# Optimization experiments

Hardware: AMD Instinct MI355X
Metric: run time of the kernel (lower is better)

## Reference

```python
import jax, jax.numpy as jnp
import numpy as np
import math

B, N, E, H = 2, 1024, 768, 12
D = E // H  # head_size = 64


def setup_inputs() -> dict:
    key = jax.random.key(0)
    ks = jax.random.split(key, 12)
    node_features = jax.random.normal(ks[0], (B, N, E), dtype=jnp.float32)
    adj = jax.random.bernoulli(ks[1], 0.5, (B, N, N))
    # ensure every row has at least one edge (self-loop) to avoid NaN softmax rows
    adj = adj | jnp.eye(N, dtype=bool)[None]
    key_edge_features = jax.random.normal(ks[2], (B, N, N, D), dtype=jnp.float32)
    s = 1.0 / math.sqrt(E)
    Wq = jax.random.normal(ks[3], (E, E), dtype=jnp.float32) * s
    bq = jnp.zeros((E,), dtype=jnp.float32)
    Wk = jax.random.normal(ks[4], (E, E), dtype=jnp.float32) * s
    bk = jnp.zeros((E,), dtype=jnp.float32)
    Wv = jax.random.normal(ks[5], (E, E), dtype=jnp.float32) * s
    bv = jnp.zeros((E,), dtype=jnp.float32)
    Wo = jax.random.normal(ks[6], (E, E), dtype=jnp.float32) * s
    bo = jnp.zeros((E,), dtype=jnp.float32)
    return dict(node_features=node_features, adj=adj, key_edge_features=key_edge_features,
                Wq=Wq, bq=bq, Wk=Wk, bk=bk, Wv=Wv, bv=bv, Wo=Wo, bo=bo)


def _heads(x):
    # (B, N, E) -> (B, H, N, D)
    return x.reshape(B, N, H, D).transpose(0, 2, 1, 3)


def reference(node_features, adj, key_edge_features, Wq, bq, Wk, bk, Wv, bv, Wo, bo):
    Q = _heads(node_features @ Wq.T + bq)  # (B,H,N,D)
    K = _heads(node_features @ Wk.T + bk)
    V = _heads(node_features @ Wv.T + bv)
    scores = jnp.einsum('bhnd,bhmd->bhnm', Q, K)
    scores = scores + jnp.einsum('bhnd,bnmd->bhnm', Q, key_edge_features)
    scores = scores / jnp.sqrt(jnp.float32(E))  # NOTE: sqrt(embed_dim), faithful to source
    scores = jnp.where(adj[:, None, :, :], scores, -jnp.inf)
    probs = jax.nn.softmax(scores, axis=-1)
    out = jnp.einsum('bhnm,bhmd->bhnd', probs, V)  # (B,H,N,D)
    out = out.transpose(0, 2, 1, 3).reshape(B, N, E)
    return out @ Wo.T + bo
```

## Files before the change

### kernel.cpp

```cpp
#include <hip/hip_runtime.h>
#include <hip/hip_bf16.h>
#include <cstdint>

typedef __attribute__((ext_vector_type(8))) short s16x8;
typedef __attribute__((ext_vector_type(8))) unsigned short u16x8_t;
typedef __attribute__((ext_vector_type(4))) float f32x4_t;
typedef __attribute__((ext_vector_type(4))) unsigned int u32x4_t;
typedef __attribute__((ext_vector_type(4))) unsigned short u16x4_t;

__device__ __forceinline__ unsigned short f2b(float f){
  unsigned u = __float_as_uint(f);
  u += 0x7fffu + ((u>>16)&1u);
  return (unsigned short)(u>>16);
}
__device__ __forceinline__ float b2f(unsigned short s){
  return __uint_as_float(((unsigned)s)<<16);
}
__device__ __forceinline__ unsigned cvt_pk_bf16(float lo, float hi){
  unsigned r;
  asm("v_cvt_pk_bf16_f32 %0, %1, %2" : "=v"(r) : "v"(lo), "v"(hi));
  return r;
}

constexpr float INV_SQRT_E = 0.036084391824351615f;
constexpr float LOG2E = 1.4426950408889634f;

__global__ void k_convert(const float* __restrict__ X,
                          const float* __restrict__ Wq, const float* __restrict__ Wk,
                          const float* __restrict__ Wv, const float* __restrict__ Wo,
                          unsigned short* __restrict__ Xb, unsigned short* __restrict__ Wst){
  const int64_t WTOT = (int64_t)3072*768/4;
  const int64_t XTOT = (int64_t)2048*768/4;
  for (int64_t i = (int64_t)blockIdx.x*blockDim.x + threadIdx.x; i < WTOT+XTOT;
       i += (int64_t)gridDim.x*blockDim.x){
    const float* src; unsigned short* dst;
    if (i < WTOT){
      int64_t e4 = i*4;
      int j = (int)(e4/768), k = (int)(e4 - (int64_t)j*768);
      int w = j/768; int jr = j - w*768;
      const float* Wsel = (w==0)? Wq : (w==1)? Wk : (w==2)? Wv : Wo;
      src = Wsel + (int64_t)jr*768 + k;
      dst = Wst + e4;
    } else {
      int64_t t = (i-WTOT)*4;
      src = X + t; dst = Xb + t;
    }
    f32x4_t v = *reinterpret_cast<const f32x4_t*>(src);
    u16x4_t o;
    o[0]=f2b(v[0]); o[1]=f2b(v[1]); o[2]=f2b(v[2]); o[3]=f2b(v[3]);
    *reinterpret_cast<u16x4_t*>(dst) = o;
  }
}

__launch_bounds__(256)
__global__ void k_gemm(const unsigned short* __restrict__ A,
                       const unsigned short* __restrict__ Wst,
                       const int mode,
                       const float* __restrict__ bq, const float* __restrict__ bk,
                       const float* __restrict__ bv, const float* __restrict__ bo,
                       unsigned short* __restrict__ Qb, unsigned short* __restrict__ Kb,
                       unsigned short* __restrict__ Vt, float* __restrict__ Out){
  __shared__ unsigned short As[64*64];
  __shared__ unsigned short Bs[64*64];
  const int tiles_n = (mode==0)?36:12;
  const int tm = blockIdx.x / tiles_n, tn = blockIdx.x % tiles_n;
  const int row0 = tm*64, col0 = tn*64;
  const unsigned short* Bbase = Wst + (mode==0 ? 0 : (int64_t)2304*768);
  const int tid = threadIdx.x;
  const int lane = tid & 63, wvi = tid >> 6;
  const int l15 = lane & 15, lg = lane >> 4;
  const int wr = (wvi>>1)*32, wc = (wvi&1)*32;
  f32x4_t acc[2][2] = {};
  for (int k0=0;k0<768;k0+=64){
    #pragma unroll
    for (int i=0;i<2;i++){
      int t = tid + i*256;
      int r = t>>3, c8 = t&7;
      u32x4_t va = *reinterpret_cast<const u32x4_t*>(A + (int64_t)(row0+r)*768 + k0 + c8*8);
      u32x4_t vb = *reinterpret_cast<const u32x4_t*>(Bbase + (int64_t)(col0+r)*768 + k0 + c8*8);
      int byt = (t*16) ^ ((r&7)<<4);
      *reinterpret_cast<u32x4_t*>(reinterpret_cast<char*>(As)+byt) = va;
      *reinterpret_cast<u32x4_t*>(reinterpret_cast<char*>(Bs)+byt) = vb;
    }
    __syncthreads();
    #pragma unroll
    for (int ks=0;ks<2;ks++){
      s16x8 af[2], bf[2];
      #pragma unroll
      for (int mt=0;mt<2;mt++){
        int r = wr + mt*16 + l15;
        int byt = (r*128 + ks*64 + lg*16) ^ ((r&7)<<4);
        af[mt] = *reinterpret_cast<const s16x8*>(reinterpret_cast<const char*>(As)+byt);
      }
      #pragma unroll
      for (int nt=0;nt<2;nt++){
        int r = wc + nt*16 + l15;
        int byt = (r*128 + ks*64 + lg*16) ^ ((r&7)<<4);
        bf[nt] = *reinterpret_cast<const s16x8*>(reinterpret_cast<const char*>(Bs)+byt);
      }
      #pragma unroll
      for (int mt=0;mt<2;mt++)
        #pragma unroll
        for (int nt=0;nt<2;nt++)
          acc[mt][nt] = __builtin_amdgcn_mfma_f32_16x16x32_bf16(af[mt], bf[nt], acc[mt][nt], 0,0,0);
    }
    __syncthreads();
  }
  #pragma unroll
  for (int mt=0;mt<2;mt++){
    #pragma unroll
    for (int nt=0;nt<2;nt++){
      int j = col0 + wc + nt*16 + l15;
      #pragma unroll
      for (int r=0;r<4;r++){
        int ii = row0 + wr + mt*16 + lg*4 + r;
        float v = acc[mt][nt][r];
        if (mode==0){
          int w = j/768; int e = j - w*768; int h = e>>6, d = e&63;
          int b = ii>>10, n = ii & 1023;
          if (w==0)      Qb[(((int64_t)(b*12+h)*1024)+n)*64+d] = f2b((v + bq[e])*INV_SQRT_E);
          else if (w==1) Kb[(((int64_t)(b*12+h)*1024)+n)*64+d] = f2b(v + bk[e]);
          else           Vt[(((int64_t)(b*12+h)*64)+d)*1024+n] = f2b(v + bv[e]);
        } else {
          Out[(int64_t)ii*768 + j] = v + bo[j];
        }
      }
    }
  }
}

__launch_bounds__(256,2)
__global__ void k_fused(const unsigned short* __restrict__ Qb, const unsigned short* __restrict__ Kb,
                        const unsigned short* __restrict__ Vt, const int* __restrict__ adj,
                        const float* __restrict__ Ef,
                        float* __restrict__ Onum, float* __restrict__ Lws){
  __shared__ float Sk[12][16][36];
  __shared__ unsigned short Sq[16][12][48];
  __shared__ unsigned short Pb[12][16][32];
  const int bid = blockIdx.x;
  const int mh = bid & 7, qt = (bid>>3) & 63, b = bid >> 9;
  const int q0 = qt*16, mbase = mh*128;
  const int tid = threadIdx.x, lane = tid & 63, wvi = tid>>6;
  const int l15 = lane & 15, lg = lane >> 4;
  const int eq = lane >> 2, mg = lane & 3;

  s16x8 afQ[3][2];
  const unsigned short* vB[3];
  const unsigned short* kB[3];
  #pragma unroll
  for (int hh=0;hh<3;hh++){
    const int h = wvi*3+hh;
    const unsigned short* p = Qb + (((int64_t)(b*12+h)*1024) + q0 + l15)*64;
    afQ[hh][0] = *reinterpret_cast<const s16x8*>(p + lg*8);
    afQ[hh][1] = *reinterpret_cast<const s16x8*>(p + 32 + lg*8);
    vB[hh]  = Vt + ((int64_t)(b*12+h)*64)*1024 + mbase + lg*8;
    kB[hh]  = Kb + ((int64_t)(b*12+h)*1024 + mbase + l15)*64;
  }
  s16x8 bfQ[4][2];
  #pragma unroll
  for (int qq=0;qq<4;qq++){
    s16x8 v0 = {}; s16x8 v1 = {};
    if (l15 < 12){
      const unsigned short* p = Qb + (((int64_t)(b*12+l15)*1024) + q0 + wvi*4 + qq)*64;
      v0 = *reinterpret_cast<const s16x8*>(p + lg*8);
      v1 = *reinterpret_cast<const s16x8*>(p + 32 + lg*8);
    }
    bfQ[qq][0]=v0; bfQ[qq][1]=v1;
  }
  const float* efBase = Ef + (((int64_t)b*1024 + q0 + wvi*4)*1024 + mbase + l15)*64 + lg*8;
  const int*  adjBase = adj + ((int64_t)b*1024 + q0 + wvi*4)*1024 + mbase + lg*4;

  f32x4_t accO[3][4] = {};
  float Lp[3] = {0.f,0.f,0.f};

  for (int step=0; step<4; step++){
    const int so = step*32;
    if (step) __syncthreads();
    s16x8 vC[3][4];
    #pragma unroll
    for (int hh=0;hh<3;hh++)
      #pragma unroll
      for (int dsb=0;dsb<4;dsb++)
        vC[hh][dsb] = *reinterpret_cast<const s16x8*>(vB[hh] + (int64_t)(dsb*16+l15)*1024 + so);
    #pragma unroll
    for (int hh=0;hh<3;hh++){
      const int h = wvi*3+hh;
      const unsigned short* kp = kB[hh] + so*64;
      #pragma unroll
      for (int mh2=0;mh2<2;mh2++){
        const unsigned short* kr = kp + mh2*16*64;
        f32x4_t a = {0.f,0.f,0.f,0.f};
        s16x8 k0v = *reinterpret_cast<const s16x8*>(kr + lg*8);
        s16x8 k1v = *reinterpret_cast<const s16x8*>(kr + 32 + lg*8);
        a = __builtin_amdgcn_mfma_f32_16x16x32_bf16(afQ[hh][0], k0v, a, 0,0,0);
        a = __builtin_amdgcn_mfma_f32_16x16x32_bf16(afQ[hh][1], k1v, a, 0,0,0);
        #pragma unroll
        for (int r=0;r<4;r++) Sk[h][lg*4+r][mh2*16+l15] = a[r];
      }
    }
    #pragma unroll
    for (int qq=0;qq<4;qq++){
      const float* ep = efBase + (int64_t)qq*65536 + so*64;
      #pragma unroll
      for (int mt2=0;mt2<2;mt2++){
        const float* e = ep + mt2*1024;
        f32x4_t acc = {0.f,0.f,0.f,0.f};
        #pragma unroll
        for (int ks=0;ks<2;ks++){
          f32x4_t lo = *reinterpret_cast<const f32x4_t*>(e + ks*32);
          f32x4_t hi = *reinterpret_cast<const f32x4_t*>(e + ks*32 + 4);
          u32x4_t ec;
          ec[0]=cvt_pk_bf16(lo[0],lo[1]); ec[1]=cvt_pk_bf16(lo[2],lo[3]);
          ec[2]=cvt_pk_bf16(hi[0],hi[1]); ec[3]=cvt_pk_bf16(hi[2],hi[3]);
          s16x8 ea = __builtin_bit_cast(s16x8, ec);
          acc = __builtin_amdgcn_mfma_f32_16x16x32_bf16(ea, bfQ[qq][ks], acc, 0,0,0);
        }
        u32x4_t av = *reinterpret_cast<const u32x4_t*>(adjBase + qq*1024 + so + mt2*16);
        if (l15 < 12){
          u16x4_t o;
          o[0] = av[0] ? f2b(acc[0]) : (unsigned short)0xFF80;
          o[1] = av[1] ? f2b(acc[1]) : (unsigned short)0xFF80;
          o[2] = av[2] ? f2b(acc[2]) : (unsigned short)0xFF80;
          o[3] = av[3] ? f2b(acc[3]) : (unsigned short)0xFF80;
          *reinterpret_cast<u16x4_t*>(&Sq[wvi*4+qq][l15][mt2*16 + lg*4]) = o;
        }
      }
    }
    __syncthreads();
    #pragma unroll
    for (int hh=0;hh<3;hh++){
      const int h = wvi*3+hh;
      const float* sr = &Sk[h][eq][mg*8];
      f32x4_t s0 = *reinterpret_cast<const f32x4_t*>(sr);
      f32x4_t s1 = *reinterpret_cast<const f32x4_t*>(sr+4);
      u16x8_t sq = *reinterpret_cast<const u16x8_t*>(&Sq[eq][h][mg*8]);
      float p[8];
      #pragma unroll
      for (int j=0;j<4;j++) p[j]   = exp2f((s0[j] + b2f(sq[j]))*LOG2E);
      #pragma unroll
      for (int j=0;j<4;j++) p[4+j] = exp2f((s1[j] + b2f(sq[4+j]))*LOG2E);
      Lp[hh] += ((p[0]+p[1])+(p[2]+p[3])) + ((p[4]+p[5])+(p[6]+p[7]));
      u32x4_t pk;
      pk[0]=cvt_pk_bf16(p[0],p[1]); pk[1]=cvt_pk_bf16(p[2],p[3]);
      pk[2]=cvt_pk_bf16(p[4],p[5]); pk[3]=cvt_pk_bf16(p[6],p[7]);
      *reinterpret_cast<u32x4_t*>(&Pb[h][eq][mg*8]) = pk;
    }
    #pragma unroll
    for (int hh=0;hh<3;hh++){
      const int h = wvi*3+hh;
      s16x8 pa = *reinterpret_cast<const s16x8*>(&Pb[h][l15][lg*8]);
      #pragma unroll
      for (int dsb=0;dsb<4;dsb++)
        accO[hh][dsb] = __builtin_amdgcn_mfma_f32_16x16x32_bf16(pa, vC[hh][dsb], accO[hh][dsb], 0,0,0);
    }
  }
  float* obase = Onum + (int64_t)(b*8+mh)*12*1024*64;
  #pragma unroll
  for (int hh=0;hh<3;hh++){
    const int h = wvi*3+hh;
    #pragma unroll
    for (int dsb=0;dsb<4;dsb++){
      #pragma unroll
      for (int r=0;r<4;r++)
        obase[((int64_t)h*1024 + q0 + lg*4 + r)*64 + dsb*16 + l15] = accO[hh][dsb][r];
    }
  }
  #pragma unroll
  for (int hh=0;hh<3;hh++){
    float Lr = Lp[hh];
    Lr += __shfl_xor(Lr, 1);
    Lr += __shfl_xor(Lr, 2);
    if (mg==0){
      int64_t idx = (((int64_t)(b*8+mh)*12)+(wvi*3+hh))*1024 + q0 + eq;
      Lws[idx] = Lr;
    }
  }
}

__global__ void k_combine(const float* __restrict__ Onum, const float* __restrict__ Lws,
                          unsigned short* __restrict__ A2){
  int64_t t = (int64_t)blockIdx.x*blockDim.x + threadIdx.x;
  if (t >= (int64_t)2*12*1024*64) return;
  const int d = (int)(t & 63);
  const int n = (int)((t>>6) & 1023);
  const int hb = (int)(t>>16);
  const int h = hb % 12, b = hb / 12;
  float num = 0.f, L = 0.f;
  #pragma unroll
  for (int p=0;p<8;p++){
    int64_t base = (((int64_t)(b*8+p)*12)+h)*1024 + n;
    L   += Lws[base];
    num += Onum[base*64 + d];
  }
  A2[((int64_t)(b*1024+n))*768 + h*64 + d] = f2b(num/L);
}

extern "C" void kernel_launch(void* const* d_in, const int* in_sizes, int n_in,
                              void* d_out, int out_size, void* d_ws, size_t ws_size,
                              hipStream_t stream){
  const float* X  = (const float*)d_in[0];
  const int*   adj= (const int*)d_in[1];
  const float* Ef = (const float*)d_in[2];
  const float* Wq = (const float*)d_in[3];
  const float* bq = (const float*)d_in[4];
  const float* Wk = (const float*)d_in[5];
  const float* bk = (const float*)d_in[6];
  const float* Wv = (const float*)d_in[7];
  const float* bv = (const float*)d_in[8];
  const float* Wo = (const float*)d_in[9];
  const float* bo = (const float*)d_in[10];
  char* w = (char*)d_ws;
  unsigned short* Xb = (unsigned short*)(w);
  unsigned short* Wst= (unsigned short*)(w + 3145728);
  unsigned short* Qb = (unsigned short*)(w + 7864320);
  unsigned short* Kb = (unsigned short*)(w + 11010048);
  unsigned short* Vt = (unsigned short*)(w + 14155776);
  float* Onum        = (float*)(w + 67633152);
  float* Lws         = (float*)(w + 117964800);
  unsigned short* A2 = (unsigned short*)(w + 118751232);
  float* Out = (float*)d_out;

  k_convert<<<3840,256,0,stream>>>(X,Wq,Wk,Wv,Wo,Xb,Wst);
  k_gemm<<<1152,256,0,stream>>>(Xb,Wst,0,bq,bk,bv,bo,Qb,Kb,Vt,nullptr);
  k_fused<<<1024,256,0,stream>>>(Qb,Kb,Vt,adj,Ef,Onum,Lws);
  k_combine<<<6144,256,0,stream>>>(Onum,Lws,A2);
  k_gemm<<<384,256,0,stream>>>(A2,Wst,1,bq,bk,bv,bo,nullptr,nullptr,nullptr,Out);
}
```

Measured before the change: 239.5 us.

## Cut LDS and registers in fused attention to allow three blocks per CU

Raises launch bounds from 2 to 3 blocks per CU. To fit that, the separate P buffer is removed: probabilities are written back in place into the Sq shared array, whose padding shrinks from 48 to 36. V fragments are now loaded just before their MFMA instead of being prefetched at the start of each step, which lowers register pressure. The aim is more resident waves to hide memory latency, at the cost of exposing V load latency right before the PV MFMAs and of possible spills under the tighter register budget.

```diff
diff --git a/kernel.cpp b/kernel.cpp
--- a/kernel.cpp
+++ b/kernel.cpp
@@ -6,6 +6,7 @@
 typedef __attribute__((ext_vector_type(8))) unsigned short u16x8_t;
 typedef __attribute__((ext_vector_type(4))) float f32x4_t;
 typedef __attribute__((ext_vector_type(4))) unsigned int u32x4_t;
+typedef __attribute__((ext_vector_type(2))) unsigned int u32x2_t;
 typedef __attribute__((ext_vector_type(4))) unsigned short u16x4_t;
 
 __device__ __forceinline__ unsigned short f2b(float f){
@@ -16,6 +17,8 @@
 __device__ __forceinline__ float b2f(unsigned short s){
   return __uint_as_float(((unsigned)s)<<16);
 }
+__device__ __forceinline__ float b2f_lo(unsigned u){ return __uint_as_float(u<<16); }
+__device__ __forceinline__ float b2f_hi(unsigned u){ return __uint_as_float(u & 0xffff0000u); }
 __device__ __forceinline__ unsigned cvt_pk_bf16(float lo, float hi){
   unsigned r;
   asm("v_cvt_pk_bf16_f32 %0, %1, %2" : "=v"(r) : "v"(lo), "v"(hi));
@@ -129,14 +132,13 @@
   }
 }
 
-__launch_bounds__(256,2)
+__launch_bounds__(256,3)
 __global__ void k_fused(const unsigned short* __restrict__ Qb, const unsigned short* __restrict__ Kb,
                         const unsigned short* __restrict__ Vt, const int* __restrict__ adj,
                         const float* __restrict__ Ef,
                         float* __restrict__ Onum, float* __restrict__ Lws){
   __shared__ float Sk[12][16][36];
-  __shared__ unsigned short Sq[16][12][48];
-  __shared__ unsigned short Pb[12][16][32];
+  __shared__ unsigned short Sq[16][12][36];
   const int bid = blockIdx.x;
   const int mh = bid & 7, qt = (bid>>3) & 63, b = bid >> 9;
   const int q0 = qt*16, mbase = mh*128;
@@ -176,12 +178,6 @@
   for (int step=0; step<4; step++){
     const int so = step*32;
     if (step) __syncthreads();
-    s16x8 vC[3][4];
-    #pragma unroll
-    for (int hh=0;hh<3;hh++)
-      #pragma unroll
-      for (int dsb=0;dsb<4;dsb++)
-        vC[hh][dsb] = *reinterpret_cast<const s16x8*>(vB[hh] + (int64_t)(dsb*16+l15)*1024 + so);
     #pragma unroll
     for (int hh=0;hh<3;hh++){
       const int h = wvi*3+hh;
@@ -233,25 +229,38 @@
       const float* sr = &Sk[h][eq][mg*8];
       f32x4_t s0 = *reinterpret_cast<const f32x4_t*>(sr);
       f32x4_t s1 = *reinterpret_cast<const f32x4_t*>(sr+4);
-      u16x8_t sq = *reinterpret_cast<const u16x8_t*>(&Sq[eq][h][mg*8]);
+      unsigned short* sqp = &Sq[eq][h][mg*8];
+      u32x2_t sq0 = *reinterpret_cast<const u32x2_t*>(sqp);
+      u32x2_t sq1 = *reinterpret_cast<const u32x2_t*>(sqp+4);
       float p[8];
-      #pragma unroll
-      for (int j=0;j<4;j++) p[j]   = exp2f((s0[j] + b2f(sq[j]))*LOG2E);
-      #pragma unroll
-      for (int j=0;j<4;j++) p[4+j] = exp2f((s1[j] + b2f(sq[4+j]))*LOG2E);
+      p[0] = exp2f((s0[0] + b2f_lo(sq0[0]))*LOG2E);
+      p[1] = exp2f((s0[1] + b2f_hi(sq0[0]))*LOG2E);
+      p[2] = exp2f((s0[2] + b2f_lo(sq0[1]))*LOG2E);
+      p[3] = exp2f((s0[3] + b2f_hi(sq0[1]))*LOG2E);
+      p[4] = exp2f((s1[0] + b2f_lo(sq1[0]))*LOG2E);
+      p[5] = exp2f((s1[1] + b2f_hi(sq1[0]))*LOG2E);
+      p[6] = exp2f((s1[2] + b2f_lo(sq1[1]))*LOG2E);
+      p[7] = exp2f((s1[3] + b2f_hi(sq1[1]))*LOG2E);
       Lp[hh] += ((p[0]+p[1])+(p[2]+p[3])) + ((p[4]+p[5])+(p[6]+p[7]));
-      u32x4_t pk;
-      pk[0]=cvt_pk_bf16(p[0],p[1]); pk[1]=cvt_pk_bf16(p[2],p[3]);
-      pk[2]=cvt_pk_bf16(p[4],p[5]); pk[3]=cvt_pk_bf16(p[6],p[7]);
-      *reinterpret_cast<u32x4_t*>(&Pb[h][eq][mg*8]) = pk;
+      u32x2_t w0; w0[0]=cvt_pk_bf16(p[0],p[1]); w0[1]=cvt_pk_bf16(p[2],p[3]);
+      *reinterpret_cast<u32x2_t*>(sqp) = w0;
+      u32x2_t w1; w1[0]=cvt_pk_bf16(p[4],p[5]); w1[1]=cvt_pk_bf16(p[6],p[7]);
+      *reinterpret_cast<u32x2_t*>(sqp+4) = w1;
     }
     #pragma unroll
     for (int hh=0;hh<3;hh++){
       const int h = wvi*3+hh;
-      s16x8 pa = *reinterpret_cast<const s16x8*>(&Pb[h][l15][lg*8]);
-      #pragma unroll
-      for (int dsb=0;dsb<4;dsb++)
-        accO[hh][dsb] = __builtin_amdgcn_mfma_f32_16x16x32_bf16(pa, vC[hh][dsb], accO[hh][dsb], 0,0,0);
+      const unsigned short* pq = &Sq[l15][h][lg*8];
+      u32x2_t a0 = *reinterpret_cast<const u32x2_t*>(pq);
+      u32x2_t a1 = *reinterpret_cast<const u32x2_t*>(pq+4);
+      u32x4_t pk4; pk4[0]=a0[0]; pk4[1]=a0[1]; pk4[2]=a1[0]; pk4[3]=a1[1];
+      s16x8 pa = __builtin_bit_cast(s16x8, pk4);
+      const unsigned short* vp = vB[hh] + so;
+      #pragma unroll
+      for (int dsb=0;dsb<4;dsb++){
+        s16x8 vb = *reinterpret_cast<const s16x8*>(vp + (int64_t)(dsb*16+l15)*1024);
+        accO[hh][dsb] = __builtin_amdgcn_mfma_f32_16x16x32_bf16(pa, vb, accO[hh][dsb], 0,0,0);
+      }
     }
   }
   float* obase = Onum + (int64_t)(b*8+mh)*12*1024*64;
```

New measurement: 264.2 us. 10.3% more time.
